# Optimization experiments

Hardware: AMD Instinct MI355X
Metric: run time of the kernel (lower is better)

## Reference

```python
import jax, jax.numpy as jnp
import numpy as np

NUM_HEADS = 8
NUM_GROUPS = 32
EPS = 1e-5


def group_norm(x, gamma, beta):
    B, C, H, W = x.shape
    xg = x.reshape(B, NUM_GROUPS, C // NUM_GROUPS * H * W)
    mean = xg.mean(axis=-1, keepdims=True)
    var = xg.var(axis=-1, keepdims=True)
    xg = (xg - mean) * jax.lax.rsqrt(var + EPS)
    xn = xg.reshape(B, C, H, W)
    return xn * gamma[None, :, None, None] + beta[None, :, None, None]


def setup_inputs() -> dict:
    key = jax.random.key(0)
    ks = jax.random.split(key, 7)
    C = 512
    B, H, W = 8, 32, 32
    x = jax.random.normal(ks[0], (B, C, H, W), dtype=jnp.float32)
    gamma = jnp.ones((C,), dtype=jnp.float32)
    beta = jnp.zeros((C,), dtype=jnp.float32)
    # 1x1 conv weights stored as [out, in]
    w_qkv = jax.random.normal(ks[1], (3 * C, C), dtype=jnp.float32) * (1.0 / np.sqrt(C))
    b_qkv = jax.random.normal(ks[2], (3 * C,), dtype=jnp.float32) * 0.02
    w_proj = jax.random.normal(ks[3], (C, C), dtype=jnp.float32) * (1.0 / np.sqrt(C))
    b_proj = jax.random.normal(ks[4], (C,), dtype=jnp.float32) * 0.02
    return {"x": x, "gamma": gamma, "beta": beta, "w_qkv": w_qkv,
            "b_qkv": b_qkv, "w_proj": w_proj, "b_proj": b_proj}


def reference(x, gamma, beta, w_qkv, b_qkv, w_proj, b_proj):
    B, C, H, W = x.shape
    hd = C // NUM_HEADS  # head_dim
    x_norm = group_norm(x, gamma, beta)
    # 1x1 conv: [B,C,H,W] x [3C,C] -> [B,3C,H,W]
    qkv = jnp.einsum('bchw,oc->bohw', x_norm, w_qkv) + b_qkv[None, :, None, None]
    q, k, v = jnp.split(qkv, 3, axis=1)
    N = H * W
    q = q.reshape(B, NUM_HEADS, hd, N)
    k = k.reshape(B, NUM_HEADS, hd, N)
    v = v.reshape(B, NUM_HEADS, hd, N)
    attn = jnp.einsum('bhcn,bhcm->bhnm', q, k) * (hd ** -0.5)
    attn = jax.nn.softmax(attn, axis=-1)
    out = jnp.einsum('bhnm,bhcm->bhcn', attn, v)
    out = out.reshape(B, C, H, W)
    proj = jnp.einsum('bchw,oc->bohw', out, w_proj) + b_proj[None, :, None, None]
    return x + proj
```

## Files before the change

### kernel.cpp

```cpp
#include <hip/hip_runtime.h>
#include <hip/hip_bf16.h>

#define BB 8
#define CC 512
#define NN 1024
#define NG 32
#define CPG 16
#define NH 8
#define HD 64
#define C3 1536
#define QKLD 1024

typedef __hip_bfloat16 bf16;
typedef unsigned short ushort_t;

typedef __attribute__((ext_vector_type(8))) short bf16x8;
typedef __attribute__((ext_vector_type(8))) unsigned short ushortx8;
typedef __attribute__((ext_vector_type(4))) float floatx4;

__device__ __forceinline__ float b2f(bf16 h) { return __bfloat162float(h); }
__device__ __forceinline__ bf16 f2b(float f) { return __float2bfloat16(f); }
__device__ __forceinline__ ushort_t f2us(float f) {
    bf16 h = __float2bfloat16(f);
    return *(ushort_t*)&h;
}

#define GLD16(gsrc, ldst)                                                        \
    __builtin_amdgcn_global_load_lds(                                            \
        (const __attribute__((address_space(1))) unsigned int*)(const void*)(gsrc), \
        (__attribute__((address_space(3))) unsigned int*)(void*)(ldst), 16, 0, 0)

__global__ __launch_bounds__(256) void gn_kernel(const float* __restrict__ x,
                                                 const float* __restrict__ gamma,
                                                 const float* __restrict__ beta,
                                                 bf16* __restrict__ xnT,
                                                 const float* __restrict__ wqkv,
                                                 const float* __restrict__ wproj,
                                                 ushort_t* __restrict__ wqkvB,
                                                 ushort_t* __restrict__ wprojB) {
    int tid = threadIdx.x;
    if (blockIdx.x >= 256) {
        int wb = blockIdx.x - 256;
        const float* src;
        ushort_t* dst;
        int base;
        if (wb < 192) { src = wqkv; dst = wqkvB; base = wb * 4096; }
        else          { src = wproj; dst = wprojB; base = (wb - 192) * 4096; }
        int o = base + tid * 4;
#pragma unroll
        for (int it = 0; it < 4; ++it) {
            float4 f = *(const float4*)(src + o + it * 1024);
            ushort_t u[4] = {f2us(f.x), f2us(f.y), f2us(f.z), f2us(f.w)};
            *(uint2*)(dst + o + it * 1024) = *(uint2*)u;
        }
        return;
    }

    const int GSZ = CPG * NN;
    int b = blockIdx.x >> 5;
    int g = blockIdx.x & 31;
    size_t base = ((size_t)b * CC + (size_t)g * CPG) * NN;

    int c_loc = tid >> 4;
    int nsp   = (tid & 15) * 16;
    const float* srcrow = x + base + (size_t)c_loc * NN;

    float fv[4][16];
    float s = 0.f, s2 = 0.f;
#pragma unroll
    for (int nc = 0; nc < 4; ++nc) {
        int nb = nc * 256 + nsp;
        *(float4*)(fv[nc] + 0)  = *(const float4*)(srcrow + nb + 0);
        *(float4*)(fv[nc] + 4)  = *(const float4*)(srcrow + nb + 4);
        *(float4*)(fv[nc] + 8)  = *(const float4*)(srcrow + nb + 8);
        *(float4*)(fv[nc] + 12) = *(const float4*)(srcrow + nb + 12);
#pragma unroll
        for (int j = 0; j < 16; ++j) { float v = fv[nc][j]; s += v; s2 += v * v; }
    }

#pragma unroll
    for (int off = 32; off > 0; off >>= 1) {
        s  += __shfl_down(s, off, 64);
        s2 += __shfl_down(s2, off, 64);
    }
    __shared__ float rs[4], rs2[4], stat[2];
    __shared__ ushort_t Lt[16][264];
    int wid = tid >> 6, lane = tid & 63;
    if (lane == 0) { rs[wid] = s; rs2[wid] = s2; }
    __syncthreads();
    if (tid == 0) {
        float ts  = rs[0] + rs[1] + rs[2] + rs[3];
        float ts2 = rs2[0] + rs2[1] + rs2[2] + rs2[3];
        float mean = ts * (1.f / GSZ);
        float var  = ts2 * (1.f / GSZ) - mean * mean;
        stat[0] = mean;
        stat[1] = rsqrtf(var + 1e-5f);
    }
    __syncthreads();
    float mean = stat[0], inv = stat[1];

    float ga = gamma[g * CPG + c_loc];
    float be = beta[g * CPG + c_loc];

    for (int nc = 0; nc < 4; ++nc) {
        ushortx8 u0, u1;
#pragma unroll
        for (int j = 0; j < 8; ++j) {
            u0[j] = f2us((fv[nc][j]     - mean) * inv * ga + be);
            u1[j] = f2us((fv[nc][j + 8] - mean) * inv * ga + be);
        }
        *(ushortx8*)&Lt[c_loc][nsp]     = u0;
        *(ushortx8*)&Lt[c_loc][nsp + 8] = u1;
        __syncthreads();
        ushort_t o16[16];
#pragma unroll
        for (int c = 0; c < 16; ++c) o16[c] = Lt[c][tid];
        ushort_t* dst = (ushort_t*)xnT + ((size_t)b * NN + nc * 256 + tid) * CC + g * CPG;
        *(uint4*)dst       = *(const uint4*)(o16);
        *(uint4*)(dst + 8) = *(const uint4*)(o16 + 8);
        __syncthreads();
    }
}

__global__ __launch_bounds__(256) void qkv_gemm(const ushort_t* __restrict__ wB,
                                                const bf16* __restrict__ xnT,
                                                const float* __restrict__ bias,
                                                bf16* __restrict__ qkT,
                                                bf16* __restrict__ vN) {
    __shared__ ushort_t Wl[128 * 32];
    __shared__ ushort_t Xl[128 * 32];
    int b  = blockIdx.z;
    int o0 = blockIdx.y * 128;
    int n0 = blockIdx.x * 128;
    int tid = threadIdx.x;
    int wv = tid >> 6, l = tid & 63, ln = l & 15, qd = (l >> 4) & 3;
    int wm = wv >> 1, wn = wv & 1;

    int strow = wv * 32 + (l >> 2);
    int sgran = (l & 3) ^ ((l >> 2) & 3);
    const ushort_t* wsrc = wB + (size_t)(o0 + strow) * CC + sgran * 8;
    const ushort_t* xsrc = (const ushort_t*)xnT + ((size_t)b * NN + n0 + strow) * CC + sgran * 8;
    ushort_t* wl0 = &Wl[(wv * 32) * 32];
    ushort_t* wl1 = &Wl[(wv * 32 + 16) * 32];
    ushort_t* xl0 = &Xl[(wv * 32) * 32];
    ushort_t* xl1 = &Xl[(wv * 32 + 16) * 32];

    floatx4 acc[4][4];
#pragma unroll
    for (int i = 0; i < 4; ++i)
#pragma unroll
        for (int j = 0; j < 4; ++j) acc[i][j] = (floatx4){0.f, 0.f, 0.f, 0.f};

    int qs = (qd ^ (ln & 3)) * 8;

    for (int k0 = 0; k0 < CC; k0 += 32) {
        GLD16(wsrc + k0, wl0);
        GLD16(wsrc + k0 + 16 * CC, wl1);
        GLD16(xsrc + k0, xl0);
        GLD16(xsrc + k0 + 16 * CC, xl1);
        __syncthreads();
        bf16x8 af[4], bfr[4];
#pragma unroll
        for (int i = 0; i < 4; ++i)
            af[i] = *(const bf16x8*)&Wl[(wm * 64 + i * 16 + ln) * 32 + qs];
#pragma unroll
        for (int j = 0; j < 4; ++j)
            bfr[j] = *(const bf16x8*)&Xl[(wn * 64 + j * 16 + ln) * 32 + qs];
#pragma unroll
        for (int i = 0; i < 4; ++i)
#pragma unroll
            for (int j = 0; j < 4; ++j)
                acc[i][j] = __builtin_amdgcn_mfma_f32_16x16x32_bf16(af[i], bfr[j], acc[i][j], 0, 0, 0);
        __syncthreads();
    }

    if (o0 < 1024) {
#pragma unroll
        for (int i = 0; i < 4; ++i) {
            int ob = o0 + wm * 64 + i * 16 + qd * 4;
            float sc = (ob < 512) ? 0.18033688011112042f : 1.0f;
#pragma unroll
            for (int j = 0; j < 4; ++j) {
                int n = n0 + wn * 64 + j * 16 + ln;
                ushort_t pk[4];
#pragma unroll
                for (int r = 0; r < 4; ++r)
                    pk[r] = f2us((acc[i][j][r] + bias[ob + r]) * sc);
                *(uint2*)((ushort_t*)qkT + ((size_t)b * NN + n) * QKLD + ob) = *(uint2*)pk;
            }
        }
    } else {
#pragma unroll
        for (int i = 0; i < 4; ++i) {
#pragma unroll
            for (int r = 0; r < 4; ++r) {
                int o = o0 + wm * 64 + i * 16 + qd * 4 + r;
                float bb = bias[o];
                size_t rb = ((size_t)b * CC + (o - 1024)) * NN + n0 + wn * 64 + ln;
#pragma unroll
                for (int j = 0; j < 4; ++j)
                    vN[rb + j * 16] = f2b(acc[i][j][r] + bb);
            }
        }
    }
}

__global__ __launch_bounds__(256, 4) void attn_kernel(const bf16* __restrict__ qkTp,
                                                      const bf16* __restrict__ vNp,
                                                      bf16* __restrict__ aoT) {
    __shared__ ushort_t Kt[2][64 * 64];
    __shared__ ushort_t Vn[2][64 * 64];
    __shared__ ushort_t Pw[4][16 * 64];

    int h  = blockIdx.x;
    int qt = blockIdx.y;
    int bi = blockIdx.z;
    int q0 = qt * 64;
    int tid = threadIdx.x;
    int wq = tid >> 6;
    int l  = tid & 63;
    int ln = l & 15;
    int qd = (l >> 4) & 3;
    int l7 = ln & 7;
    int lb = ln >> 3;

    const ushort_t* qkT = (const ushort_t*)qkTp;
    const ushort_t* vN  = (const ushort_t*)vNp;

    const ushort_t* qsrc = qkT + ((size_t)bi * NN + q0 + wq * 16 + ln) * QKLD + h * HD + qd * 8;
    bf16x8 aq0 = *(const bf16x8*)(qsrc);
    bf16x8 aq1 = *(const bf16x8*)(qsrc + 32);

    bf16x8 ones;
#pragma unroll
    for (int j = 0; j < 8; ++j) ones[j] = (short)0x3F80;

    floatx4 O[4];
#pragma unroll
    for (int t = 0; t < 4; ++t) O[t] = (floatx4){0.f, 0.f, 0.f, 0.f};
    floatx4 lsum = (floatx4){0.f, 0.f, 0.f, 0.f};

    ushort_t* Pme = &Pw[wq][0];

    int ksl0 = (qd ^ l7) * 8;
    int ksl1 = ((qd + 4) ^ l7) * 8;

    int srow = tid >> 2;
    int g1   = tid & 3;
    int s7   = srow & 7;
    int ko1  = (g1 ^ s7) * 8;
    int ko2  = ((g1 + 4) ^ s7) * 8;
    const ushort_t* ks = qkT + ((size_t)bi * NN + srow) * QKLD + 512 + h * HD + g1 * 8;
    const ushort_t* vs = vN + ((size_t)bi * CC + h * HD + srow) * NN + g1 * 8;

    uint4 kr0 = *(const uint4*)(ks);
    uint4 kr1 = *(const uint4*)(ks + 32);
    uint4 vr0 = *(const uint4*)(vs);
    uint4 vr1 = *(const uint4*)(vs + 32);
    {
        ushort_t* kd = &Kt[0][srow * 64];
        *(uint4*)(kd + ko1) = kr0; *(uint4*)(kd + ko2) = kr1;
        ushort_t* vd = &Vn[0][srow * 64];
        *(uint4*)(vd + ko1) = vr0; *(uint4*)(vd + ko2) = vr1;
    }
    kr0 = *(const uint4*)(ks + (size_t)64 * QKLD);
    kr1 = *(const uint4*)(ks + (size_t)64 * QKLD + 32);
    vr0 = *(const uint4*)(vs + 64);
    vr1 = *(const uint4*)(vs + 64 + 32);
    __syncthreads();

    for (int it = 0; it < 16; ++it) {
        int cur = it & 1;
        const ushort_t* KtC = &Kt[cur][0];
        const ushort_t* VnC = &Vn[cur][0];
        if (it < 15) {
            ushort_t* kd = &Kt[cur ^ 1][srow * 64];
            *(uint4*)(kd + ko1) = kr0; *(uint4*)(kd + ko2) = kr1;
            ushort_t* vd = &Vn[cur ^ 1][srow * 64];
            *(uint4*)(vd + ko1) = vr0; *(uint4*)(vd + ko2) = vr1;
        }
        if (it < 14) {
            size_t mo = (size_t)(it + 2) * 64;
            kr0 = *(const uint4*)(ks + mo * QKLD);
            kr1 = *(const uint4*)(ks + mo * QKLD + 32);
            vr0 = *(const uint4*)(vs + mo);
            vr1 = *(const uint4*)(vs + mo + 32);
        }

        floatx4 S[4];
#pragma unroll
        for (int t = 0; t < 4; ++t) {
            const ushort_t* krow = KtC + (t * 16 + ln) * 64;
            bf16x8 b0 = *(const bf16x8*)(krow + ksl0);
            bf16x8 b1 = *(const bf16x8*)(krow + ksl1);
            floatx4 acc = (floatx4){0.f, 0.f, 0.f, 0.f};
            acc = __builtin_amdgcn_mfma_f32_16x16x32_bf16(aq0, b0, acc, 0, 0, 0);
            acc = __builtin_amdgcn_mfma_f32_16x16x32_bf16(aq1, b1, acc, 0, 0, 0);
            S[t] = acc;
        }

#pragma unroll
        for (int t = 0; t < 4; ++t) {
#pragma unroll
            for (int r = 0; r < 4; ++r) {
                float p = exp2f(S[t][r]);
                int qr = qd * 4 + r;
                Pme[qr * 64 + ((t * 2 + lb) ^ (qr & 7)) * 8 + l7] = f2us(p);
            }
        }
        bf16x8 pa0 = *(const bf16x8*)&Pme[ln * 64 + ksl0];
        bf16x8 pa1 = *(const bf16x8*)&Pme[ln * 64 + ksl1];

        lsum = __builtin_amdgcn_mfma_f32_16x16x32_bf16(pa0, ones, lsum, 0, 0, 0);
        lsum = __builtin_amdgcn_mfma_f32_16x16x32_bf16(pa1, ones, lsum, 0, 0, 0);

#pragma unroll
        for (int t = 0; t < 4; ++t) {
            const ushort_t* vrow = VnC + (t * 16 + ln) * 64;
            bf16x8 v0 = *(const bf16x8*)(vrow + ksl0);
            bf16x8 v1 = *(const bf16x8*)(vrow + ksl1);
            O[t] = __builtin_amdgcn_mfma_f32_16x16x32_bf16(pa0, v0, O[t], 0, 0, 0);
            O[t] = __builtin_amdgcn_mfma_f32_16x16x32_bf16(pa1, v1, O[t], 0, 0, 0);
        }
        if (it < 15) __syncthreads();
    }

    float inv[4];
#pragma unroll
    for (int r = 0; r < 4; ++r) inv[r] = 1.f / lsum[r];
#pragma unroll
    for (int t = 0; t < 4; ++t) {
#pragma unroll
        for (int r = 0; r < 4; ++r) {
            int n = q0 + wq * 16 + qd * 4 + r;
            ((ushort_t*)aoT)[((size_t)bi * NN + n) * CC + h * HD + t * 16 + ln] =
                f2us(O[t][r] * inv[r]);
        }
    }
}

__global__ __launch_bounds__(256) void proj_gemm(const bf16* __restrict__ aoT,
                                                 const ushort_t* __restrict__ wB,
                                                 const float* __restrict__ bias,
                                                 const float* __restrict__ xres,
                                                 float* __restrict__ out) {
    __shared__ ushort_t Wl[64 * 32];
    __shared__ ushort_t Xl[128 * 32];
    int b  = blockIdx.z;
    int o0 = blockIdx.y * 64;
    int n0 = blockIdx.x * 128;
    int tid = threadIdx.x;
    int wv = tid >> 6, l = tid & 63, ln = l & 15, qd = (l >> 4) & 3;
    int wm = wv >> 1, wn = wv & 1;

    int strow = wv * 32 + (l >> 2);
    int sgran = (l & 3) ^ ((l >> 2) & 3);
    const ushort_t* xsrc = (const ushort_t*)aoT + ((size_t)b * NN + n0 + strow) * CC + sgran * 8;
    int wrow = wv * 16 + (l >> 2);
    const ushort_t* wsrc = wB + (size_t)(o0 + wrow) * CC + sgran * 8;
    ushort_t* xl0 = &Xl[(wv * 32) * 32];
    ushort_t* xl1 = &Xl[(wv * 32 + 16) * 32];
    ushort_t* wl0 = &Wl[(wv * 16) * 32];

    floatx4 acc[2][4];
#pragma unroll
    for (int i = 0; i < 2; ++i)
#pragma unroll
        for (int j = 0; j < 4; ++j) acc[i][j] = (floatx4){0.f, 0.f, 0.f, 0.f};

    int qs = (qd ^ (ln & 3)) * 8;

    for (int k0 = 0; k0 < CC; k0 += 32) {
        GLD16(wsrc + k0, wl0);
        GLD16(xsrc + k0, xl0);
        GLD16(xsrc + k0 + 16 * CC, xl1);
        __syncthreads();
        bf16x8 af[2], bfr[4];
#pragma unroll
        for (int i = 0; i < 2; ++i)
            af[i] = *(const bf16x8*)&Wl[(wm * 32 + i * 16 + ln) * 32 + qs];
#pragma unroll
        for (int j = 0; j < 4; ++j)
            bfr[j] = *(const bf16x8*)&Xl[(wn * 64 + j * 16 + ln) * 32 + qs];
#pragma unroll
        for (int i = 0; i < 2; ++i)
#pragma unroll
            for (int j = 0; j < 4; ++j)
                acc[i][j] = __builtin_amdgcn_mfma_f32_16x16x32_bf16(af[i], bfr[j], acc[i][j], 0, 0, 0);
        __syncthreads();
    }

#pragma unroll
    for (int i = 0; i < 2; ++i) {
#pragma unroll
        for (int r = 0; r < 4; ++r) {
            int o = o0 + wm * 32 + i * 16 + qd * 4 + r;
            float bb = bias[o];
            size_t rb = ((size_t)b * CC + o) * NN + n0 + wn * 64 + ln;
#pragma unroll
            for (int j = 0; j < 4; ++j)
                out[rb + j * 16] = acc[i][j][r] + bb + xres[rb + j * 16];
        }
    }
}

extern "C" void kernel_launch(void* const* d_in, const int* in_sizes, int n_in,
                              void* d_out, int out_size, void* d_ws, size_t ws_size,
                              hipStream_t stream) {
    const float* x      = (const float*)d_in[0];
    const float* gamma  = (const float*)d_in[1];
    const float* beta   = (const float*)d_in[2];
    const float* w_qkv  = (const float*)d_in[3];
    const float* b_qkv  = (const float*)d_in[4];
    const float* w_proj = (const float*)d_in[5];
    const float* b_proj = (const float*)d_in[6];
    float* out = (float*)d_out;

    bf16* xnT = (bf16*)d_ws;
    bf16* qkT = xnT + (size_t)BB * CC * NN;
    bf16* vN  = qkT + (size_t)BB * NN * QKLD;
    ushort_t* wqkvB  = (ushort_t*)(vN + (size_t)BB * CC * NN);
    ushort_t* wprojB = wqkvB + (size_t)C3 * CC;
    bf16* aoT = xnT;

    gn_kernel<<<BB * NG + 256, 256, 0, stream>>>(x, gamma, beta, xnT,
                                                 w_qkv, w_proj, wqkvB, wprojB);
    qkv_gemm<<<dim3(NN / 128, C3 / 128, BB), 256, 0, stream>>>(wqkvB, xnT, b_qkv, qkT, vN);
    attn_kernel<<<dim3(NH, NN / 64, BB), 256, 0, stream>>>(qkT, vN, aoT);
    proj_gemm<<<dim3(NN / 128, CC / 64, BB), 256, 0, stream>>>(aoT, wprojB, b_proj, x, out);
}
```

Measured before the change: 163.0 us.

## Double-buffer LDS tiles in QKV and projection GEMMs to overlap loads

The QKV and projection GEMM kernels now keep two LDS buffers and issue the global-to-LDS loads for the next K slice before computing on the current one. The goal is to hide global load latency behind the MFMA work, and each iteration uses one barrier instead of two. The cost is twice the LDS per block, which may reduce occupancy. The group-norm kernel also gets launch bounds with min blocks 1 and an unrolled channel-chunk loop.

```diff
diff --git a/kernel.cpp b/kernel.cpp
--- a/kernel.cpp
+++ b/kernel.cpp
@@ -30,14 +30,14 @@
         (const __attribute__((address_space(1))) unsigned int*)(const void*)(gsrc), \
         (__attribute__((address_space(3))) unsigned int*)(void*)(ldst), 16, 0, 0)
 
-__global__ __launch_bounds__(256) void gn_kernel(const float* __restrict__ x,
-                                                 const float* __restrict__ gamma,
-                                                 const float* __restrict__ beta,
-                                                 bf16* __restrict__ xnT,
-                                                 const float* __restrict__ wqkv,
-                                                 const float* __restrict__ wproj,
-                                                 ushort_t* __restrict__ wqkvB,
-                                                 ushort_t* __restrict__ wprojB) {
+__global__ __launch_bounds__(256, 1) void gn_kernel(const float* __restrict__ x,
+                                                    const float* __restrict__ gamma,
+                                                    const float* __restrict__ beta,
+                                                    bf16* __restrict__ xnT,
+                                                    const float* __restrict__ wqkv,
+                                                    const float* __restrict__ wproj,
+                                                    ushort_t* __restrict__ wqkvB,
+                                                    ushort_t* __restrict__ wprojB) {
     int tid = threadIdx.x;
     if (blockIdx.x >= 256) {
         int wb = blockIdx.x - 256;
@@ -102,6 +102,7 @@
     float ga = gamma[g * CPG + c_loc];
     float be = beta[g * CPG + c_loc];
 
+#pragma unroll
     for (int nc = 0; nc < 4; ++nc) {
         ushortx8 u0, u1;
 #pragma unroll
@@ -127,8 +128,8 @@
                                                 const float* __restrict__ bias,
                                                 bf16* __restrict__ qkT,
                                                 bf16* __restrict__ vN) {
-    __shared__ ushort_t Wl[128 * 32];
-    __shared__ ushort_t Xl[128 * 32];
+    __shared__ ushort_t Wl[2][128 * 32];
+    __shared__ ushort_t Xl[2][128 * 32];
     int b  = blockIdx.z;
     int o0 = blockIdx.y * 128;
     int n0 = blockIdx.x * 128;
@@ -140,10 +141,8 @@
     int sgran = (l & 3) ^ ((l >> 2) & 3);
     const ushort_t* wsrc = wB + (size_t)(o0 + strow) * CC + sgran * 8;
     const ushort_t* xsrc = (const ushort_t*)xnT + ((size_t)b * NN + n0 + strow) * CC + sgran * 8;
-    ushort_t* wl0 = &Wl[(wv * 32) * 32];
-    ushort_t* wl1 = &Wl[(wv * 32 + 16) * 32];
-    ushort_t* xl0 = &Xl[(wv * 32) * 32];
-    ushort_t* xl1 = &Xl[(wv * 32 + 16) * 32];
+    int lr0 = (wv * 32) * 32;
+    int lr1 = (wv * 32 + 16) * 32;
 
     floatx4 acc[4][4];
 #pragma unroll
@@ -153,25 +152,35 @@
 
     int qs = (qd ^ (ln & 3)) * 8;
 
+    GLD16(wsrc, &Wl[0][lr0]);
+    GLD16(wsrc + 16 * CC, &Wl[0][lr1]);
+    GLD16(xsrc, &Xl[0][lr0]);
+    GLD16(xsrc + 16 * CC, &Xl[0][lr1]);
+    __syncthreads();
+
+    int cur = 0;
     for (int k0 = 0; k0 < CC; k0 += 32) {
-        GLD16(wsrc + k0, wl0);
-        GLD16(wsrc + k0 + 16 * CC, wl1);
-        GLD16(xsrc + k0, xl0);
-        GLD16(xsrc + k0 + 16 * CC, xl1);
-        __syncthreads();
+        int nxt = cur ^ 1;
+        if (k0 + 32 < CC) {
+            GLD16(wsrc + k0 + 32, &Wl[nxt][lr0]);
+            GLD16(wsrc + k0 + 32 + 16 * CC, &Wl[nxt][lr1]);
+            GLD16(xsrc + k0 + 32, &Xl[nxt][lr0]);
+            GLD16(xsrc + k0 + 32 + 16 * CC, &Xl[nxt][lr1]);
+        }
         bf16x8 af[4], bfr[4];
 #pragma unroll
         for (int i = 0; i < 4; ++i)
-            af[i] = *(const bf16x8*)&Wl[(wm * 64 + i * 16 + ln) * 32 + qs];
+            af[i] = *(const bf16x8*)&Wl[cur][(wm * 64 + i * 16 + ln) * 32 + qs];
 #pragma unroll
         for (int j = 0; j < 4; ++j)
-            bfr[j] = *(const bf16x8*)&Xl[(wn * 64 + j * 16 + ln) * 32 + qs];
+            bfr[j] = *(const bf16x8*)&Xl[cur][(wn * 64 + j * 16 + ln) * 32 + qs];
 #pragma unroll
         for (int i = 0; i < 4; ++i)
 #pragma unroll
             for (int j = 0; j < 4; ++j)
                 acc[i][j] = __builtin_amdgcn_mfma_f32_16x16x32_bf16(af[i], bfr[j], acc[i][j], 0, 0, 0);
         __syncthreads();
+        cur = nxt;
     }
 
     if (o0 < 1024) {
@@ -344,8 +353,8 @@
                                                  const float* __restrict__ bias,
                                                  const float* __restrict__ xres,
                                                  float* __restrict__ out) {
-    __shared__ ushort_t Wl[64 * 32];
-    __shared__ ushort_t Xl[128 * 32];
+    __shared__ ushort_t Wl[2][64 * 32];
+    __shared__ ushort_t Xl[2][128 * 32];
     int b  = blockIdx.z;
     int o0 = blockIdx.y * 64;
     int n0 = blockIdx.x * 128;
@@ -358,9 +367,9 @@
     const ushort_t* xsrc = (const ushort_t*)aoT + ((size_t)b * NN + n0 + strow) * CC + sgran * 8;
     int wrow = wv * 16 + (l >> 2);
     const ushort_t* wsrc = wB + (size_t)(o0 + wrow) * CC + sgran * 8;
-    ushort_t* xl0 = &Xl[(wv * 32) * 32];
-    ushort_t* xl1 = &Xl[(wv * 32 + 16) * 32];
-    ushort_t* wl0 = &Wl[(wv * 16) * 32];
+    int xr0 = (wv * 32) * 32;
+    int xr1 = (wv * 32 + 16) * 32;
+    int wr0 = (wv * 16) * 32;
 
     floatx4 acc[2][4];
 #pragma unroll
@@ -370,24 +379,33 @@
 
     int qs = (qd ^ (ln & 3)) * 8;
 
+    GLD16(wsrc, &Wl[0][wr0]);
+    GLD16(xsrc, &Xl[0][xr0]);
+    GLD16(xsrc + 16 * CC, &Xl[0][xr1]);
+    __syncthreads();
+
+    int cur = 0;
     for (int k0 = 0; k0 < CC; k0 += 32) {
-        GLD16(wsrc + k0, wl0);
-        GLD16(xsrc + k0, xl0);
-        GLD16(xsrc + k0 + 16 * CC, xl1);
-        __syncthreads();
+        int nxt = cur ^ 1;
+        if (k0 + 32 < CC) {
+            GLD16(wsrc + k0 + 32, &Wl[nxt][wr0]);
+            GLD16(xsrc + k0 + 32, &Xl[nxt][xr0]);
+            GLD16(xsrc + k0 + 32 + 16 * CC, &Xl[nxt][xr1]);
+        }
         bf16x8 af[2], bfr[4];
 #pragma unroll
         for (int i = 0; i < 2; ++i)
-            af[i] = *(const bf16x8*)&Wl[(wm * 32 + i * 16 + ln) * 32 + qs];
+            af[i] = *(const bf16x8*)&Wl[cur][(wm * 32 + i * 16 + ln) * 32 + qs];
 #pragma unroll
         for (int j = 0; j < 4; ++j)
-            bfr[j] = *(const bf16x8*)&Xl[(wn * 64 + j * 16 + ln) * 32 + qs];
+            bfr[j] = *(const bf16x8*)&Xl[cur][(wn * 64 + j * 16 + ln) * 32 + qs];
 #pragma unroll
         for (int i = 0; i < 2; ++i)
 #pragma unroll
             for (int j = 0; j < 4; ++j)
                 acc[i][j] = __builtin_amdgcn_mfma_f32_16x16x32_bf16(af[i], bfr[j], acc[i][j], 0, 0, 0);
         __syncthreads();
+        cur = nxt;
     }
 
 #pragma unroll
```

Result: no change. 163.2 us (+0.1%).
